# Performance work log

Hardware: AMD Instinct MI355X
Metric: run time of the kernel (lower is better)

The kernel has to match this reference:

```python
import jax, jax.numpy as jnp
import numpy as np

N_NODES = 50000
N_EDGES = 800000
N_GRAPHS = 64


def graph_conv(x, edge_index, w_rel, b_rel, w_root):
    # PyG GraphConv with aggr='add':
    #   out = lin_rel(sum_{j in N(i)} x_j) + lin_root(x_i)
    src, dst = edge_index[0], edge_index[1]
    agg = jax.ops.segment_sum(x[src], dst, num_segments=x.shape[0])  # [N, d_in]
    return agg @ w_rel + b_rel + x @ w_root  # [N, d_out]


def scatter_mean(x, batch, num_segments):
    s = jax.ops.segment_sum(x, batch, num_segments=num_segments)
    cnt = jax.ops.segment_sum(jnp.ones((x.shape[0],), x.dtype), batch,
                              num_segments=num_segments)
    return s / jnp.maximum(cnt, 1.0)[:, None]


def setup_inputs() -> dict:
    key = jax.random.key(0)
    ks = jax.random.split(key, 8)
    d_feat, d_hid, d_out = 128, 128, 128
    x = jax.random.normal(ks[0], (N_NODES, d_feat), dtype=jnp.float32)
    edge_index = jax.random.randint(ks[1], (2, N_EDGES), 0, N_NODES, dtype=jnp.int64)
    batch = jnp.sort(jax.random.randint(ks[2], (N_NODES,), 0, N_GRAPHS, dtype=jnp.int64))

    def glorot(k, shape):
        fan_in = shape[0]
        return jax.random.normal(k, shape, dtype=jnp.float32) / np.sqrt(fan_in)

    return {
        "x": x,
        "edge_index": edge_index,
        "batch": batch,
        "w_rel1": glorot(ks[3], (d_feat, d_hid)),
        "b_rel1": jnp.zeros((d_hid,), jnp.float32),
        "w_root1": glorot(ks[4], (d_feat, d_hid)),
        "w_rel2": glorot(ks[5], (d_hid, 2 * d_hid)),
        "b_rel2": jnp.zeros((2 * d_hid,), jnp.float32),
        "w_root2": glorot(ks[6], (d_hid, 2 * d_hid)),
        "w_rel3": glorot(ks[7], (2 * d_hid, d_out)),
        "b_rel3": jnp.zeros((d_out,), jnp.float32),
        "w_root3": glorot(jax.random.fold_in(key, 99), (2 * d_hid, d_out)),
    }


def reference(x, edge_index, batch,
              w_rel1, b_rel1, w_root1,
              w_rel2, b_rel2, w_root2,
              w_rel3, b_rel3, w_root3):
    h = jax.nn.elu(graph_conv(x, edge_index, w_rel1, b_rel1, w_root1))
    h = jax.nn.elu(graph_conv(h, edge_index, w_rel2, b_rel2, w_root2))
    h = jax.nn.elu(graph_conv(h, edge_index, w_rel3, b_rel3, w_root3))
    return scatter_mean(h, batch, N_GRAPHS)  # [num_graphs, n_out]
```

## Files before the change

### kernel.cpp

```cpp
#include <hip/hip_runtime.h>
#include <math.h>

#define NN 50000
#define NNP 50048
#define NE 800000
#define NG 64
#define NBK 196
#define ECH 4082
#define TOTH (NBK * NBK)
#define NBH 151
#define SBLK 6890
#define SWORK (NN * 32 + 163840)

typedef __attribute__((ext_vector_type(8))) __bf16 bf16x8;
typedef __attribute__((ext_vector_type(4))) float f32x4;

__device__ inline unsigned short f2bf(float f) {
    unsigned int u = __float_as_uint(f);
    u += 0x7fffu + ((u >> 16) & 1u);
    return (unsigned short)(u >> 16);
}
__device__ inline float bflo(unsigned int v) { return __uint_as_float(v << 16); }
__device__ inline float bfhi(unsigned int v) { return __uint_as_float(v & 0xffff0000u); }
__device__ inline float bfs(unsigned short v) { return __uint_as_float((unsigned int)v << 16); }

#define GLD_LDS16(g, l)                                                          \
    __builtin_amdgcn_global_load_lds(                                            \
        (const __attribute__((address_space(1))) unsigned int*)(g),              \
        (__attribute__((address_space(3))) unsigned int*)(l), 16, 0, 0)

__global__ __launch_bounds__(256) void front_k(const float* __restrict__ x,
                                               const float* __restrict__ wr1,
                                               const float* __restrict__ wo1,
                                               const float* __restrict__ wr2,
                                               const float* __restrict__ wo2,
                                               const float* __restrict__ wr3,
                                               const float* __restrict__ wo3,
                                               const int* __restrict__ edst,
                                               const int* __restrict__ batch,
                                               unsigned short* __restrict__ xb,
                                               unsigned short* __restrict__ W1T,
                                               unsigned short* __restrict__ W2T,
                                               unsigned short* __restrict__ W3T,
                                               int* __restrict__ H,
                                               int* __restrict__ bounds,
                                               float* __restrict__ outp) {
    const int b = blockIdx.x, t = threadIdx.x;
    if (b < SBLK) {
        int id = b * 256 + t;
        if (id < NN * 32) {
            float4 v = ((const float4*)x)[id];
            unsigned int p0 = ((unsigned int)f2bf(v.y) << 16) | f2bf(v.x);
            unsigned int p1 = ((unsigned int)f2bf(v.w) << 16) | f2bf(v.z);
            ((uint2*)xb)[id] = make_uint2(p0, p1);
            return;
        }
        int w = id - NN * 32;
        if (w < 32768) {
            int n = w >> 8, k = w & 255;
            W1T[w] = f2bf((k < 128) ? wr1[k * 128 + n] : wo1[(k - 128) * 128 + n]);
        } else if (w < 98304) {
            int j = w - 32768; int n = j >> 8, k = j & 255;
            W2T[j] = f2bf((k < 128) ? wr2[k * 256 + n] : wo2[(k - 128) * 256 + n]);
        } else if (w < 163840) {
            int j = w - 98304; int n = j >> 8, k = j & 255;
            W3T[j] = f2bf((n < 128) ? wr3[k * 128 + n] : wo3[k * 128 + (n - 128)]);
        }
        return;
    }
    if (b < SBLK + NBK) {
        __shared__ int h[NBK];
        int k = b - SBLK;
        if (t < NBK) h[t] = 0;
        __syncthreads();
        int e0 = k * ECH, e1 = min(NE, e0 + ECH);
        for (int e = e0 + t; e < e1; e += 256) atomicAdd(&h[edst[e] >> 8], 1);
        __syncthreads();
        if (t < NBK) H[t * NBK + k] = h[t];
        return;
    }
    if (t <= NG) {
        int g = t, lo = 0, hi = NN;
        while (lo < hi) { int mid = (lo + hi) >> 1; if (batch[mid] < g) lo = mid + 1; else hi = mid; }
        bounds[g] = lo;
    }
    for (int i = t; i < NG * 128; i += 256) outp[i] = 0.f;
}

__global__ __launch_bounds__(256) void hsum_k(const int* __restrict__ H,
                                              int* __restrict__ hb) {
    int i = blockIdx.x * 256 + threadIdx.x;
    int v = (i < TOTH) ? H[i] : 0;
    for (int off = 32; off; off >>= 1) v += __shfl_xor(v, off, 64);
    __shared__ int ws[4];
    if ((threadIdx.x & 63) == 0) ws[threadIdx.x >> 6] = v;
    __syncthreads();
    if (threadIdx.x == 0) hb[blockIdx.x] = ws[0] + ws[1] + ws[2] + ws[3];
}

__global__ __launch_bounds__(256) void happly_k(const int* __restrict__ H,
                                                const int* __restrict__ hb,
                                                int* __restrict__ S) {
    __shared__ int s[256], ws[4], choff;
    const int t = threadIdx.x, c = blockIdx.x;
    {
        int v = (t < c) ? hb[t] : 0;
        for (int off = 32; off; off >>= 1) v += __shfl_xor(v, off, 64);
        if ((t & 63) == 0) ws[t >> 6] = v;
        __syncthreads();
        if (t == 0) choff = ws[0] + ws[1] + ws[2] + ws[3];
        __syncthreads();
    }
    int i = c * 256 + t;
    int v = (i < TOTH) ? H[i] : 0;
    s[t] = v; __syncthreads();
    for (int off = 1; off < 256; off <<= 1) {
        int u = (t >= off) ? s[t - off] : 0;
        __syncthreads(); s[t] += u; __syncthreads();
    }
    if (i < TOTH) S[i] = choff + s[t] - v;
}

__global__ __launch_bounds__(256) void scatter_k(const int* __restrict__ src,
                                                 const int* __restrict__ dst,
                                                 const int* __restrict__ S,
                                                 int* __restrict__ tmp) {
    __shared__ int cur[NBK];
    int t = threadIdx.x, k = blockIdx.x;
    if (t < NBK) cur[t] = S[t * NBK + k];
    __syncthreads();
    int e0 = k * ECH, e1 = min(NE, e0 + ECH);
    for (int e = e0 + t; e < e1; e += 256) {
        int d = dst[e];
        int p = atomicAdd(&cur[d >> 8], 1);
        tmp[p] = ((d & 255) << 16) | src[e];
    }
}

__global__ __launch_bounds__(256) void csr_k(const int* __restrict__ tmp,
                                             const int* __restrict__ S,
                                             int* __restrict__ rowptr,
                                             int* __restrict__ colsrc) {
    __shared__ int hist[256], off[256], cur[256];
    int t = threadIdx.x, b = blockIdx.x;
    int base = S[b * NBK];
    int next = (b < NBK - 1) ? S[(b + 1) * NBK] : NE;
    int cntb = next - base;
    hist[t] = 0;
    __syncthreads();
    for (int i = t; i < cntb; i += 256) atomicAdd(&hist[tmp[base + i] >> 16], 1);
    __syncthreads();
    int v = hist[t];
    off[t] = v; __syncthreads();
    for (int o = 1; o < 256; o <<= 1) {
        int u = (t >= o) ? off[t - o] : 0;
        __syncthreads(); off[t] += u; __syncthreads();
    }
    int excl = off[t] - v;
    int node = b * 256 + t;
    if (node <= NN) rowptr[node] = base + excl;
    cur[t] = excl;
    __syncthreads();
    for (int i = t; i < cntb; i += 256) {
        int e = tmp[base + i];
        int p = atomicAdd(&cur[e >> 16], 1);
        colsrc[base + p] = e & 0xffff;
    }
}

__global__ __launch_bounds__(256) void aggb_k(const unsigned short* __restrict__ feat,
                                              const int* __restrict__ rowptr,
                                              const int* __restrict__ colsrc,
                                              unsigned short* __restrict__ outp) {
    const int node = __builtin_amdgcn_readfirstlane((int)(blockIdx.x * 4 + (threadIdx.x >> 6)));
    const int lane = threadIdx.x & 63;
    const int half = lane >> 5, l32 = lane & 31;
    const int beg = rowptr[node], end = rowptr[node + 1];
    float a0 = 0.f, a1 = 0.f, a2 = 0.f, a3 = 0.f;
    int e = beg;
    for (; e + 16 <= end; e += 16) {
        int c[8]; uint2 v[8];
#pragma unroll
        for (int i = 0; i < 8; ++i) c[i] = colsrc[e + 2 * i + half];
#pragma unroll
        for (int i = 0; i < 8; ++i)
            v[i] = *(const uint2*)&feat[(size_t)c[i] * 128 + l32 * 4];
#pragma unroll
        for (int i = 0; i < 8; ++i) {
            a0 += bflo(v[i].x); a1 += bfhi(v[i].x);
            a2 += bflo(v[i].y); a3 += bfhi(v[i].y);
        }
    }
    for (; e + 4 <= end; e += 4) {
        int c[2]; uint2 v[2];
#pragma unroll
        for (int i = 0; i < 2; ++i) c[i] = colsrc[e + 2 * i + half];
#pragma unroll
        for (int i = 0; i < 2; ++i)
            v[i] = *(const uint2*)&feat[(size_t)c[i] * 128 + l32 * 4];
#pragma unroll
        for (int i = 0; i < 2; ++i) {
            a0 += bflo(v[i].x); a1 += bfhi(v[i].x);
            a2 += bflo(v[i].y); a3 += bfhi(v[i].y);
        }
    }
    if (e + 2 <= end) {
        int c = colsrc[e + half];
        uint2 v = *(const uint2*)&feat[(size_t)c * 128 + l32 * 4];
        a0 += bflo(v.x); a1 += bfhi(v.x); a2 += bflo(v.y); a3 += bfhi(v.y);
        e += 2;
    }
    if (e < end && half == 0) {
        int c = colsrc[e];
        uint2 v = *(const uint2*)&feat[(size_t)c * 128 + l32 * 4];
        a0 += bflo(v.x); a1 += bfhi(v.x); a2 += bflo(v.y); a3 += bfhi(v.y);
    }
    a0 += __shfl_xor(a0, 32, 64);
    a1 += __shfl_xor(a1, 32, 64);
    a2 += __shfl_xor(a2, 32, 64);
    a3 += __shfl_xor(a3, 32, 64);
    if (half == 0) {
        unsigned int p0 = ((unsigned int)f2bf(a1) << 16) | f2bf(a0);
        unsigned int p1 = ((unsigned int)f2bf(a3) << 16) | f2bf(a2);
        *(uint2*)&outp[(size_t)node * 128 + l32 * 4] = make_uint2(p0, p1);
    }
}

__global__ __launch_bounds__(256) void aggf_k(const unsigned short* __restrict__ y,
                                              const unsigned short* __restrict__ rr,
                                              const float* __restrict__ b3,
                                              const int* __restrict__ rowptr,
                                              const int* __restrict__ colsrc,
                                              unsigned short* __restrict__ outp) {
    const int node = __builtin_amdgcn_readfirstlane((int)(blockIdx.x * 4 + (threadIdx.x >> 6)));
    const int lane = threadIdx.x & 63;
    const int half = lane >> 5, l32 = lane & 31;
    const int beg = rowptr[node], end = rowptr[node + 1];
    float a0 = 0.f, a1 = 0.f, a2 = 0.f, a3 = 0.f;
    int e = beg;
    for (; e + 16 <= end; e += 16) {
        int c[8]; uint2 v[8];
#pragma unroll
        for (int i = 0; i < 8; ++i) c[i] = colsrc[e + 2 * i + half];
#pragma unroll
        for (int i = 0; i < 8; ++i)
            v[i] = *(const uint2*)&y[(size_t)c[i] * 128 + l32 * 4];
#pragma unroll
        for (int i = 0; i < 8; ++i) {
            a0 += bflo(v[i].x); a1 += bfhi(v[i].x);
            a2 += bflo(v[i].y); a3 += bfhi(v[i].y);
        }
    }
    for (; e + 4 <= end; e += 4) {
        int c[2]; uint2 v[2];
#pragma unroll
        for (int i = 0; i < 2; ++i) c[i] = colsrc[e + 2 * i + half];
#pragma unroll
        for (int i = 0; i < 2; ++i)
            v[i] = *(const uint2*)&y[(size_t)c[i] * 128 + l32 * 4];
#pragma unroll
        for (int i = 0; i < 2; ++i) {
            a0 += bflo(v[i].x); a1 += bfhi(v[i].x);
            a2 += bflo(v[i].y); a3 += bfhi(v[i].y);
        }
    }
    if (e + 2 <= end) {
        int c = colsrc[e + half];
        uint2 v = *(const uint2*)&y[(size_t)c * 128 + l32 * 4];
        a0 += bflo(v.x); a1 += bfhi(v.x); a2 += bflo(v.y); a3 += bfhi(v.y);
        e += 2;
    }
    if (e < end && half == 0) {
        int c = colsrc[e];
        uint2 v = *(const uint2*)&y[(size_t)c * 128 + l32 * 4];
        a0 += bflo(v.x); a1 += bfhi(v.x); a2 += bflo(v.y); a3 += bfhi(v.y);
    }
    a0 += __shfl_xor(a0, 32, 64);
    a1 += __shfl_xor(a1, 32, 64);
    a2 += __shfl_xor(a2, 32, 64);
    a3 += __shfl_xor(a3, 32, 64);
    if (half == 0) {
        uint2 rv = *(const uint2*)&rr[(size_t)node * 128 + l32 * 4];
        float4 bb = *(const float4*)&b3[l32 * 4];
        float v0 = a0 + bflo(rv.x) + bb.x;
        float v1 = a1 + bfhi(rv.x) + bb.y;
        float v2 = a2 + bflo(rv.y) + bb.z;
        float v3 = a3 + bfhi(rv.y) + bb.w;
        v0 = v0 > 0.f ? v0 : (__expf(v0) - 1.f);
        v1 = v1 > 0.f ? v1 : (__expf(v1) - 1.f);
        v2 = v2 > 0.f ? v2 : (__expf(v2) - 1.f);
        v3 = v3 > 0.f ? v3 : (__expf(v3) - 1.f);
        unsigned int p0 = ((unsigned int)f2bf(v1) << 16) | f2bf(v0);
        unsigned int p1 = ((unsigned int)f2bf(v3) << 16) | f2bf(v2);
        *(uint2*)&outp[(size_t)node * 128 + l32 * 4] = make_uint2(p0, p1);
    }
}

template <bool TWO, int N, bool BIAS, bool ELU, bool SPLIT>
__global__ __launch_bounds__(256) void gemmB_k(const unsigned short* __restrict__ A1,
                                               const unsigned short* __restrict__ A2,
                                               const unsigned short* __restrict__ WT,
                                               const float* __restrict__ bias,
                                               unsigned short* __restrict__ Cout,
                                               unsigned short* __restrict__ Cout2) {
    constexpr int AST = TWO ? 128 : 256;
    constexpr int NH = N / 2;
    constexpr int NI = NH / 16;
    constexpr int SIT = N / 16;
    __shared__ __attribute__((aligned(16))) unsigned short Bs[N * 128];

    const int t = threadIdx.x;
    const int wv = t >> 6, lane = t & 63;
    const int qd = lane >> 4, l16 = lane & 15;
    const int m0 = blockIdx.x * 64;
    const int mrow = m0 + (wv >> 1) * 32 + l16;
    const int nb = (wv & 1) * NH;
    const int swz = (t & 15) ^ (t >> 4);

    f32x4 acc[2][NI] = {};
    bf16x8 av[2][2];

    auto stageB = [&](int p) {
#pragma unroll
        for (int i = 0; i < SIT; ++i) {
            int row = i * 16 + (t >> 4);
            const unsigned short* g = WT + (size_t)row * 256 + p * 128 + swz * 8;
            GLD_LDS16(g, &Bs[i * 2048 + t * 8]);
        }
    };
    auto loadA = [&](int ks, int d) {
        const unsigned short* base = (TWO && ks >= 4) ? A2 : A1;
        int kc = TWO ? ((ks & 3) * 32) : (ks * 32);
        av[d][0] = *(const bf16x8*)&base[(size_t)mrow * AST + kc + qd * 8];
        av[d][1] = *(const bf16x8*)&base[(size_t)(mrow + 16) * AST + kc + qd * 8];
    };
    auto kstep = [&](int ks, int d) {
        int ksl = ks & 3;
        bf16x8 bfr[NI];
#pragma unroll
        for (int ni = 0; ni < NI; ++ni) {
            int row = nb + ni * 16 + l16;
            int slot = (ksl * 4 + qd) ^ l16;
            bfr[ni] = *(const bf16x8*)&Bs[row * 128 + slot * 8];
        }
#pragma unroll
        for (int mi = 0; mi < 2; ++mi)
#pragma unroll
            for (int ni = 0; ni < NI; ++ni)
                acc[mi][ni] = __builtin_amdgcn_mfma_f32_16x16x32_bf16(
                    av[d][mi], bfr[ni], acc[mi][ni], 0, 0, 0);
    };

    stageB(0);
    asm volatile("" ::: "memory");
    loadA(0, 0);
    asm volatile("s_waitcnt vmcnt(2)" ::: "memory");
    __builtin_amdgcn_s_barrier();
    loadA(1, 1); kstep(0, 0);
    loadA(2, 0); kstep(1, 1);
    loadA(3, 1); kstep(2, 0);
    kstep(3, 1);
    asm volatile("s_waitcnt lgkmcnt(0)" ::: "memory");
    __builtin_amdgcn_s_barrier();
    stageB(1);
    asm volatile("" ::: "memory");
    loadA(4, 0);
    asm volatile("s_waitcnt vmcnt(2)" ::: "memory");
    __builtin_amdgcn_s_barrier();
    loadA(5, 1); kstep(4, 0);
    loadA(6, 0); kstep(5, 1);
    loadA(7, 1); kstep(6, 0);
    kstep(7, 1);

#pragma unroll
    for (int mi = 0; mi < 2; ++mi)
#pragma unroll
        for (int ni = 0; ni < NI; ++ni)
#pragma unroll
            for (int r = 0; r < 4; ++r) {
                int mm = m0 + (wv >> 1) * 32 + mi * 16 + qd * 4 + r;
                if (mm < NN) {
                    int nn = nb + ni * 16 + l16;
                    float v = acc[mi][ni][r];
                    if (BIAS) v += bias[nn];
                    if (ELU) v = v > 0.f ? v : (__expf(v) - 1.f);
                    unsigned short bv = f2bf(v);
                    if (SPLIT) {
                        unsigned short* dst = (nn < 128) ? Cout : Cout2;
                        dst[(size_t)mm * 128 + (nn & 127)] = bv;
                    } else {
                        Cout[(size_t)mm * N + nn] = bv;
                    }
                }
            }
}

__global__ __launch_bounds__(256) void sum_k(const unsigned short* __restrict__ vals,
                                             const int* __restrict__ batch,
                                             float* __restrict__ outsum) {
    const int CH = 25;
    int wv = threadIdx.x >> 6, lane = threadIdx.x & 63;
    int n0 = (blockIdx.x * 4 + wv) * CH;
    int g = batch[n0];
    float ax = 0.f, ay = 0.f;
    for (int i = 0; i < CH; ++i) {
        int n = n0 + i;
        int gn = batch[n];
        if (gn != g) {
            unsafeAtomicAdd(&outsum[(size_t)g * 128 + lane * 2], ax);
            unsafeAtomicAdd(&outsum[(size_t)g * 128 + lane * 2 + 1], ay);
            ax = 0.f; ay = 0.f; g = gn;
        }
        unsigned int v = *(const unsigned int*)&vals[(size_t)n * 128 + lane * 2];
        ax += bflo(v); ay += bfhi(v);
    }
    unsafeAtomicAdd(&outsum[(size_t)g * 128 + lane * 2], ax);
    unsafeAtomicAdd(&outsum[(size_t)g * 128 + lane * 2 + 1], ay);
}

__global__ void divide_k(const int* __restrict__ bounds, float* __restrict__ out) {
    int i = blockIdx.x * 256 + threadIdx.x;
    if (i < NG * 128) {
        int g = i >> 7;
        float c = (float)(bounds[g + 1] - bounds[g]);
        out[i] /= fmaxf(c, 1.f);
    }
}

extern "C" void kernel_launch(void* const* d_in, const int* in_sizes, int n_in,
                              void* d_out, int out_size, void* d_ws, size_t ws_size,
                              hipStream_t stream) {
    const float* x       = (const float*)d_in[0];
    const int*   ei      = (const int*)d_in[1];
    const int*   batch   = (const int*)d_in[2];
    const float* w_rel1  = (const float*)d_in[3];
    const float* b_rel1  = (const float*)d_in[4];
    const float* w_root1 = (const float*)d_in[5];
    const float* w_rel2  = (const float*)d_in[6];
    const float* b_rel2  = (const float*)d_in[7];
    const float* w_root2 = (const float*)d_in[8];
    const float* w_rel3  = (const float*)d_in[9];
    const float* b_rel3  = (const float*)d_in[10];
    const float* w_root3 = (const float*)d_in[11];
    const int* esrc = ei;
    const int* edst = ei + NE;

    unsigned short* Ab = (unsigned short*)d_ws;
    unsigned short* Bb = Ab + (size_t)NNP * 128;
    unsigned short* Cb = Bb + (size_t)NNP * 128;
    unsigned short* xb = Cb + (size_t)NNP * 256;
    unsigned short* W1T = xb + (size_t)NNP * 128;
    unsigned short* W2T = W1T + 128 * 256;
    unsigned short* W3T = W2T + 256 * 256;
    int* rowptr = (int*)(W3T + 256 * 256);
    int* colsrc = rowptr + (NN + 1);
    int* tmp    = colsrc + NE;
    int* H      = tmp + NE;
    int* S      = H + TOTH;
    int* hb     = S + TOTH;
    int* bounds = hb + 256;
    float* outp = (float*)d_out;

    front_k<<<SBLK + NBK + 1, 256, 0, stream>>>(
        x, w_rel1, w_root1, w_rel2, w_root2, w_rel3, w_root3, edst, batch,
        xb, W1T, W2T, W3T, H, bounds, outp);
    hsum_k<<<NBH, 256, 0, stream>>>(H, hb);
    happly_k<<<NBH, 256, 0, stream>>>(H, hb, S);
    scatter_k<<<NBK, 256, 0, stream>>>(esrc, edst, S, tmp);
    csr_k<<<NBK, 256, 0, stream>>>(tmp, S, rowptr, colsrc);

    aggb_k<<<NN / 4, 256, 0, stream>>>(xb, rowptr, colsrc, Ab);
    gemmB_k<true, 128, true, true, false>
        <<<NNP / 64, 256, 0, stream>>>(Ab, xb, W1T, b_rel1, Bb, nullptr);

    aggb_k<<<NN / 4, 256, 0, stream>>>(Bb, rowptr, colsrc, Ab);
    gemmB_k<true, 256, true, true, false>
        <<<NNP / 64, 256, 0, stream>>>(Ab, Bb, W2T, b_rel2, Cb, nullptr);

    gemmB_k<false, 256, false, false, true>
        <<<NNP / 64, 256, 0, stream>>>(Cb, nullptr, W3T, nullptr, Ab, Bb);

    aggf_k<<<NN / 4, 256, 0, stream>>>(Ab, Bb, b_rel3, rowptr, colsrc, Cb);
    sum_k<<<NN / 100, 256, 0, stream>>>(Cb, batch, outp);
    divide_k<<<(NG * 128 + 255) / 256, 256, 0, stream>>>(bounds, outp);
}
```

Measured before the change: 305.1 us.

## Slice node features into 32-column slabs for cache-friendly gather aggregation

Features are additionally written in a slab layout of four 32-column slices per node, and the aggregation kernels launch one block per node group per slice. Each block gathers only a 64-byte slice per neighbor, so the working set of each slice pass fits better in L2/MALL. Non-temporal loads and stores are used for colsrc and the outputs. The cost is extra slab writes in front_k and the GEMM epilogues, four times as many aggregation blocks, and reading colsrc four times.

```diff
diff --git a/kernel.cpp b/kernel.cpp
--- a/kernel.cpp
+++ b/kernel.cpp
@@ -39,6 +39,7 @@
                                                const int* __restrict__ edst,
                                                const int* __restrict__ batch,
                                                unsigned short* __restrict__ xb,
+                                               unsigned short* __restrict__ xs,
                                                unsigned short* __restrict__ W1T,
                                                unsigned short* __restrict__ W2T,
                                                unsigned short* __restrict__ W3T,
@@ -53,6 +54,9 @@
             unsigned int p0 = ((unsigned int)f2bf(v.y) << 16) | f2bf(v.x);
             unsigned int p1 = ((unsigned int)f2bf(v.w) << 16) | f2bf(v.z);
             ((uint2*)xb)[id] = make_uint2(p0, p1);
+            int row = id >> 5, c4 = (id & 31) << 2;
+            *(uint2*)&xs[((size_t)(c4 >> 5) * NNP + row) * 32 + (c4 & 31)] =
+                make_uint2(p0, p1);
             return;
         }
         int w = id - NN * 32;
@@ -168,141 +172,108 @@
     }
 }
 
-__global__ __launch_bounds__(256) void aggb_k(const unsigned short* __restrict__ feat,
+__global__ __launch_bounds__(256) void agg4_k(const unsigned short* __restrict__ slabs,
                                               const int* __restrict__ rowptr,
                                               const int* __restrict__ colsrc,
                                               unsigned short* __restrict__ outp) {
-    const int node = __builtin_amdgcn_readfirstlane((int)(blockIdx.x * 4 + (threadIdx.x >> 6)));
+    const int slice = blockIdx.x & 3;
+    const int node = __builtin_amdgcn_readfirstlane(
+        (int)((blockIdx.x >> 2) * 4 + (threadIdx.x >> 6)));
     const int lane = threadIdx.x & 63;
-    const int half = lane >> 5, l32 = lane & 31;
+    const int sub = lane >> 4, fl = lane & 15;
+    const unsigned short* feat = slabs + (size_t)slice * NNP * 32;
+    const int fo = fl * 2;
     const int beg = rowptr[node], end = rowptr[node + 1];
-    float a0 = 0.f, a1 = 0.f, a2 = 0.f, a3 = 0.f;
+    float a0 = 0.f, a1 = 0.f;
     int e = beg;
     for (; e + 16 <= end; e += 16) {
-        int c[8]; uint2 v[8];
-#pragma unroll
-        for (int i = 0; i < 8; ++i) c[i] = colsrc[e + 2 * i + half];
-#pragma unroll
-        for (int i = 0; i < 8; ++i)
-            v[i] = *(const uint2*)&feat[(size_t)c[i] * 128 + l32 * 4];
-#pragma unroll
-        for (int i = 0; i < 8; ++i) {
-            a0 += bflo(v[i].x); a1 += bfhi(v[i].x);
-            a2 += bflo(v[i].y); a3 += bfhi(v[i].y);
-        }
+        int c[4]; unsigned int v[4];
+#pragma unroll
+        for (int i = 0; i < 4; ++i) c[i] = __builtin_nontemporal_load(&colsrc[e + 4 * i + sub]);
+#pragma unroll
+        for (int i = 0; i < 4; ++i)
+            v[i] = *(const unsigned int*)&feat[(size_t)c[i] * 32 + fo];
+#pragma unroll
+        for (int i = 0; i < 4; ++i) { a0 += bflo(v[i]); a1 += bfhi(v[i]); }
     }
     for (; e + 4 <= end; e += 4) {
-        int c[2]; uint2 v[2];
-#pragma unroll
-        for (int i = 0; i < 2; ++i) c[i] = colsrc[e + 2 * i + half];
-#pragma unroll
-        for (int i = 0; i < 2; ++i)
-            v[i] = *(const uint2*)&feat[(size_t)c[i] * 128 + l32 * 4];
-#pragma unroll
-        for (int i = 0; i < 2; ++i) {
-            a0 += bflo(v[i].x); a1 += bfhi(v[i].x);
-            a2 += bflo(v[i].y); a3 += bfhi(v[i].y);
-        }
-    }
-    if (e + 2 <= end) {
-        int c = colsrc[e + half];
-        uint2 v = *(const uint2*)&feat[(size_t)c * 128 + l32 * 4];
-        a0 += bflo(v.x); a1 += bfhi(v.x); a2 += bflo(v.y); a3 += bfhi(v.y);
-        e += 2;
-    }
-    if (e < end && half == 0) {
-        int c = colsrc[e];
-        uint2 v = *(const uint2*)&feat[(size_t)c * 128 + l32 * 4];
-        a0 += bflo(v.x); a1 += bfhi(v.x); a2 += bflo(v.y); a3 += bfhi(v.y);
-    }
-    a0 += __shfl_xor(a0, 32, 64);
-    a1 += __shfl_xor(a1, 32, 64);
-    a2 += __shfl_xor(a2, 32, 64);
-    a3 += __shfl_xor(a3, 32, 64);
-    if (half == 0) {
-        unsigned int p0 = ((unsigned int)f2bf(a1) << 16) | f2bf(a0);
-        unsigned int p1 = ((unsigned int)f2bf(a3) << 16) | f2bf(a2);
-        *(uint2*)&outp[(size_t)node * 128 + l32 * 4] = make_uint2(p0, p1);
-    }
-}
-
-__global__ __launch_bounds__(256) void aggf_k(const unsigned short* __restrict__ y,
-                                              const unsigned short* __restrict__ rr,
-                                              const float* __restrict__ b3,
-                                              const int* __restrict__ rowptr,
-                                              const int* __restrict__ colsrc,
-                                              unsigned short* __restrict__ outp) {
-    const int node = __builtin_amdgcn_readfirstlane((int)(blockIdx.x * 4 + (threadIdx.x >> 6)));
+        int c = __builtin_nontemporal_load(&colsrc[e + sub]);
+        unsigned int v = *(const unsigned int*)&feat[(size_t)c * 32 + fo];
+        a0 += bflo(v); a1 += bfhi(v);
+    }
+    int rem = end - e;
+    if (sub < rem) {
+        int c = __builtin_nontemporal_load(&colsrc[e + sub]);
+        unsigned int v = *(const unsigned int*)&feat[(size_t)c * 32 + fo];
+        a0 += bflo(v); a1 += bfhi(v);
+    }
+    a0 += __shfl_xor(a0, 16, 64); a1 += __shfl_xor(a1, 16, 64);
+    a0 += __shfl_xor(a0, 32, 64); a1 += __shfl_xor(a1, 32, 64);
+    if (lane < 16) {
+        unsigned int p = ((unsigned int)f2bf(a1) << 16) | f2bf(a0);
+        __builtin_nontemporal_store(p, (unsigned int*)&outp[(size_t)node * 128 + slice * 32 + fo]);
+    }
+}
+
+__global__ __launch_bounds__(256) void aggf4_k(const unsigned short* __restrict__ slabs,
+                                               const unsigned short* __restrict__ rr,
+                                               const float* __restrict__ b3,
+                                               const int* __restrict__ rowptr,
+                                               const int* __restrict__ colsrc,
+                                               unsigned short* __restrict__ outp) {
+    const int slice = blockIdx.x & 3;
+    const int node = __builtin_amdgcn_readfirstlane(
+        (int)((blockIdx.x >> 2) * 4 + (threadIdx.x >> 6)));
     const int lane = threadIdx.x & 63;
-    const int half = lane >> 5, l32 = lane & 31;
+    const int sub = lane >> 4, fl = lane & 15;
+    const unsigned short* feat = slabs + (size_t)slice * NNP * 32;
+    const int fo = fl * 2;
     const int beg = rowptr[node], end = rowptr[node + 1];
-    float a0 = 0.f, a1 = 0.f, a2 = 0.f, a3 = 0.f;
+    float a0 = 0.f, a1 = 0.f;
     int e = beg;
     for (; e + 16 <= end; e += 16) {
-        int c[8]; uint2 v[8];
-#pragma unroll
-        for (int i = 0; i < 8; ++i) c[i] = colsrc[e + 2 * i + half];
-#pragma unroll
-        for (int i = 0; i < 8; ++i)
-            v[i] = *(const uint2*)&y[(size_t)c[i] * 128 + l32 * 4];
-#pragma unroll
-        for (int i = 0; i < 8; ++i) {
-            a0 += bflo(v[i].x); a1 += bfhi(v[i].x);
-            a2 += bflo(v[i].y); a3 += bfhi(v[i].y);
-        }
+        int c[4]; unsigned int v[4];
+#pragma unroll
+        for (int i = 0; i < 4; ++i) c[i] = __builtin_nontemporal_load(&colsrc[e + 4 * i + sub]);
+#pragma unroll
+        for (int i = 0; i < 4; ++i)
+            v[i] = *(const unsigned int*)&feat[(size_t)c[i] * 32 + fo];
+#pragma unroll
+        for (int i = 0; i < 4; ++i) { a0 += bflo(v[i]); a1 += bfhi(v[i]); }
     }
     for (; e + 4 <= end; e += 4) {
-        int c[2]; uint2 v[2];
-#pragma unroll
-        for (int i = 0; i < 2; ++i) c[i] = colsrc[e + 2 * i + half];
-#pragma unroll
-        for (int i = 0; i < 2; ++i)
-            v[i] = *(const uint2*)&y[(size_t)c[i] * 128 + l32 * 4];
-#pragma unroll
-        for (int i = 0; i < 2; ++i) {
-            a0 += bflo(v[i].x); a1 += bfhi(v[i].x);
-            a2 += bflo(v[i].y); a3 += bfhi(v[i].y);
-        }
-    }
-    if (e + 2 <= end) {
-        int c = colsrc[e + half];
-        uint2 v = *(const uint2*)&y[(size_t)c * 128 + l32 * 4];
-        a0 += bflo(v.x); a1 += bfhi(v.x); a2 += bflo(v.y); a3 += bfhi(v.y);
-        e += 2;
-    }
-    if (e < end && half == 0) {
-        int c = colsrc[e];
-        uint2 v = *(const uint2*)&y[(size_t)c * 128 + l32 * 4];
-        a0 += bflo(v.x); a1 += bfhi(v.x); a2 += bflo(v.y); a3 += bfhi(v.y);
-    }
-    a0 += __shfl_xor(a0, 32, 64);
-    a1 += __shfl_xor(a1, 32, 64);
-    a2 += __shfl_xor(a2, 32, 64);
-    a3 += __shfl_xor(a3, 32, 64);
-    if (half == 0) {
-        uint2 rv = *(const uint2*)&rr[(size_t)node * 128 + l32 * 4];
-        float4 bb = *(const float4*)&b3[l32 * 4];
-        float v0 = a0 + bflo(rv.x) + bb.x;
-        float v1 = a1 + bfhi(rv.x) + bb.y;
-        float v2 = a2 + bflo(rv.y) + bb.z;
-        float v3 = a3 + bfhi(rv.y) + bb.w;
+        int c = __builtin_nontemporal_load(&colsrc[e + sub]);
+        unsigned int v = *(const unsigned int*)&feat[(size_t)c * 32 + fo];
+        a0 += bflo(v); a1 += bfhi(v);
+    }
+    int rem = end - e;
+    if (sub < rem) {
+        int c = __builtin_nontemporal_load(&colsrc[e + sub]);
+        unsigned int v = *(const unsigned int*)&feat[(size_t)c * 32 + fo];
+        a0 += bflo(v); a1 += bfhi(v);
+    }
+    a0 += __shfl_xor(a0, 16, 64); a1 += __shfl_xor(a1, 16, 64);
+    a0 += __shfl_xor(a0, 32, 64); a1 += __shfl_xor(a1, 32, 64);
+    if (lane < 16) {
+        int col = slice * 32 + fo;
+        unsigned int rv = *(const unsigned int*)&rr[(size_t)node * 128 + col];
+        float2 bb = *(const float2*)&b3[col];
+        float v0 = a0 + bflo(rv) + bb.x;
+        float v1 = a1 + bfhi(rv) + bb.y;
         v0 = v0 > 0.f ? v0 : (__expf(v0) - 1.f);
         v1 = v1 > 0.f ? v1 : (__expf(v1) - 1.f);
-        v2 = v2 > 0.f ? v2 : (__expf(v2) - 1.f);
-        v3 = v3 > 0.f ? v3 : (__expf(v3) - 1.f);
-        unsigned int p0 = ((unsigned int)f2bf(v1) << 16) | f2bf(v0);
-        unsigned int p1 = ((unsigned int)f2bf(v3) << 16) | f2bf(v2);
-        *(uint2*)&outp[(size_t)node * 128 + l32 * 4] = make_uint2(p0, p1);
-    }
-}
-
-template <bool TWO, int N, bool BIAS, bool ELU, bool SPLIT>
+        unsigned int p = ((unsigned int)f2bf(v1) << 16) | f2bf(v0);
+        __builtin_nontemporal_store(p, (unsigned int*)&outp[(size_t)node * 128 + col]);
+    }
+}
+
+template <bool TWO, int N, bool BIAS, bool ELU, int SLAB>
 __global__ __launch_bounds__(256) void gemmB_k(const unsigned short* __restrict__ A1,
                                                const unsigned short* __restrict__ A2,
                                                const unsigned short* __restrict__ WT,
                                                const float* __restrict__ bias,
                                                unsigned short* __restrict__ Cout,
-                                               unsigned short* __restrict__ Cout2) {
+                                               unsigned short* __restrict__ slab) {
     constexpr int AST = TWO ? 128 : 256;
     constexpr int NH = N / 2;
     constexpr int NI = NH / 16;
@@ -385,11 +356,15 @@
                     if (BIAS) v += bias[nn];
                     if (ELU) v = v > 0.f ? v : (__expf(v) - 1.f);
                     unsigned short bv = f2bf(v);
-                    if (SPLIT) {
-                        unsigned short* dst = (nn < 128) ? Cout : Cout2;
-                        dst[(size_t)mm * 128 + (nn & 127)] = bv;
+                    if (SLAB == 2) {
+                        if (nn < 128)
+                            slab[((size_t)(nn >> 5) * NNP + mm) * 32 + (nn & 31)] = bv;
+                        else
+                            Cout[(size_t)mm * 128 + (nn & 127)] = bv;
                     } else {
                         Cout[(size_t)mm * N + nn] = bv;
+                        if (SLAB == 1)
+                            slab[((size_t)(nn >> 5) * NNP + mm) * 32 + (nn & 31)] = bv;
                     }
                 }
             }
@@ -449,7 +424,9 @@
     unsigned short* Bb = Ab + (size_t)NNP * 128;
     unsigned short* Cb = Bb + (size_t)NNP * 128;
     unsigned short* xb = Cb + (size_t)NNP * 256;
-    unsigned short* W1T = xb + (size_t)NNP * 128;
+    unsigned short* xs = xb + (size_t)NNP * 128;
+    unsigned short* hs = xs + (size_t)NNP * 128;
+    unsigned short* W1T = hs + (size_t)NNP * 128;
     unsigned short* W2T = W1T + 128 * 256;
     unsigned short* W3T = W2T + 256 * 256;
     int* rowptr = (int*)(W3T + 256 * 256);
@@ -459,28 +436,29 @@
     int* S      = H + TOTH;
     int* hb     = S + TOTH;
     int* bounds = hb + 256;
+    unsigned short* ys = xs;
     float* outp = (float*)d_out;
 
     front_k<<<SBLK + NBK + 1, 256, 0, stream>>>(
         x, w_rel1, w_root1, w_rel2, w_root2, w_rel3, w_root3, edst, batch,
-        xb, W1T, W2T, W3T, H, bounds, outp);
+        xb, xs, W1T, W2T, W3T, H, bounds, outp);
     hsum_k<<<NBH, 256, 0, stream>>>(H, hb);
     happly_k<<<NBH, 256, 0, stream>>>(H, hb, S);
     scatter_k<<<NBK, 256, 0, stream>>>(esrc, edst, S, tmp);
     csr_k<<<NBK, 256, 0, stream>>>(tmp, S, rowptr, colsrc);
 
-    aggb_k<<<NN / 4, 256, 0, stream>>>(xb, rowptr, colsrc, Ab);
-    gemmB_k<true, 128, true, true, false>
-        <<<NNP / 64, 256, 0, stream>>>(Ab, xb, W1T, b_rel1, Bb, nullptr);
-
-    aggb_k<<<NN / 4, 256, 0, stream>>>(Bb, rowptr, colsrc, Ab);
-    gemmB_k<true, 256, true, true, false>
+    agg4_k<<<NN, 256, 0, stream>>>(xs, rowptr, colsrc, Ab);
+    gemmB_k<true, 128, true, true, 1>
+        <<<NNP / 64, 256, 0, stream>>>(Ab, xb, W1T, b_rel1, Bb, hs);
+
+    agg4_k<<<NN, 256, 0, stream>>>(hs, rowptr, colsrc, Ab);
+    gemmB_k<true, 256, true, true, 0>
         <<<NNP / 64, 256, 0, stream>>>(Ab, Bb, W2T, b_rel2, Cb, nullptr);
 
-    gemmB_k<false, 256, false, false, true>
-        <<<NNP / 64, 256, 0, stream>>>(Cb, nullptr, W3T, nullptr, Ab, Bb);
-
-    aggf_k<<<NN / 4, 256, 0, stream>>>(Ab, Bb, b_rel3, rowptr, colsrc, Cb);
+    gemmB_k<false, 256, false, false, 2>
+        <<<NNP / 64, 256, 0, stream>>>(Cb, nullptr, W3T, nullptr, Bb, ys);
+
+    aggf4_k<<<NN, 256, 0, stream>>>(ys, Bb, b_rel3, rowptr, colsrc, Cb);
     sum_k<<<NN / 100, 256, 0, stream>>>(Cb, batch, outp);
     divide_k<<<(NG * 128 + 255) / 256, 256, 0, stream>>>(bounds, outp);
 }
```

New measurement: 473.8 us. 1.55x slower.

## Restructure GEMM into 128-row tiles with full-K weight slab staged once

Applied to the files above, without the earlier changes.

Replaces the two-phase pipelined GEMM kernel with one where each block handles 128 rows and one 128-column output half, loads all K=256 of its A fragments into registers up front, and stages the entire 128x256 weight slice into LDS in a single pass. Wider outputs are split across paired blocks. The goal is fewer barriers and phase switches, and more rows reusing each staged weight tile. In exchange it uses more registers and 64KB of LDS per block, and it no longer overlaps loads with MFMA work inside a block.

```diff
diff --git a/kernel.cpp b/kernel.cpp
--- a/kernel.cpp
+++ b/kernel.cpp
@@ -10,7 +10,6 @@
 #define TOTH (NBK * NBK)
 #define NBH 151
 #define SBLK 6890
-#define SWORK (NN * 32 + 163840)
 
 typedef __attribute__((ext_vector_type(8))) __bf16 bf16x8;
 typedef __attribute__((ext_vector_type(4))) float f32x4;
@@ -296,100 +295,83 @@
     }
 }
 
-template <bool TWO, int N, bool BIAS, bool ELU, bool SPLIT>
-__global__ __launch_bounds__(256) void gemmB_k(const unsigned short* __restrict__ A1,
-                                               const unsigned short* __restrict__ A2,
-                                               const unsigned short* __restrict__ WT,
-                                               const float* __restrict__ bias,
-                                               unsigned short* __restrict__ Cout,
-                                               unsigned short* __restrict__ Cout2) {
+template <bool TWO, int NOUT, bool BIAS, bool ELU, bool SPLIT>
+__global__ __launch_bounds__(256, 2) void gemmS_k(const unsigned short* __restrict__ A1,
+                                                  const unsigned short* __restrict__ A2,
+                                                  const unsigned short* __restrict__ WT,
+                                                  const float* __restrict__ bias,
+                                                  unsigned short* __restrict__ C1,
+                                                  unsigned short* __restrict__ C2) {
+    constexpr int NH = NOUT / 128;
     constexpr int AST = TWO ? 128 : 256;
-    constexpr int NH = N / 2;
-    constexpr int NI = NH / 16;
-    constexpr int SIT = N / 16;
-    __shared__ __attribute__((aligned(16))) unsigned short Bs[N * 128];
+    __shared__ __attribute__((aligned(16))) unsigned short Ws[128 * 256];
 
     const int t = threadIdx.x;
     const int wv = t >> 6, lane = t & 63;
     const int qd = lane >> 4, l16 = lane & 15;
-    const int m0 = blockIdx.x * 64;
-    const int mrow = m0 + (wv >> 1) * 32 + l16;
-    const int nb = (wv & 1) * NH;
-    const int swz = (t & 15) ^ (t >> 4);
-
-    f32x4 acc[2][NI] = {};
-    bf16x8 av[2][2];
-
-    auto stageB = [&](int p) {
-#pragma unroll
-        for (int i = 0; i < SIT; ++i) {
-            int row = i * 16 + (t >> 4);
-            const unsigned short* g = WT + (size_t)row * 256 + p * 128 + swz * 8;
-            GLD_LDS16(g, &Bs[i * 2048 + t * 8]);
-        }
-    };
-    auto loadA = [&](int ks, int d) {
+    const int h  = (NH == 2) ? (int)(blockIdx.x & 1) : 0;
+    const int rb = (NH == 2) ? (int)(blockIdx.x >> 1) : (int)blockIdx.x;
+    const int m0 = rb * 128;
+    const int mrow = m0 + wv * 32 + l16;
+
+    bf16x8 av[16];
+#pragma unroll
+    for (int ks = 0; ks < 8; ++ks) {
         const unsigned short* base = (TWO && ks >= 4) ? A2 : A1;
-        int kc = TWO ? ((ks & 3) * 32) : (ks * 32);
-        av[d][0] = *(const bf16x8*)&base[(size_t)mrow * AST + kc + qd * 8];
-        av[d][1] = *(const bf16x8*)&base[(size_t)(mrow + 16) * AST + kc + qd * 8];
-    };
-    auto kstep = [&](int ks, int d) {
-        int ksl = ks & 3;
-        bf16x8 bfr[NI];
-#pragma unroll
-        for (int ni = 0; ni < NI; ++ni) {
-            int row = nb + ni * 16 + l16;
-            int slot = (ksl * 4 + qd) ^ l16;
-            bfr[ni] = *(const bf16x8*)&Bs[row * 128 + slot * 8];
+        const int kc = TWO ? ((ks & 3) * 32) : (ks * 32);
+        av[2 * ks]     = *(const bf16x8*)&base[(size_t)mrow * AST + kc + qd * 8];
+        av[2 * ks + 1] = *(const bf16x8*)&base[(size_t)(mrow + 16) * AST + kc + qd * 8];
+    }
+    {
+        const int rl = t >> 5;
+        const int slot = t & 31;
+#pragma unroll
+        for (int i = 0; i < 16; ++i) {
+            int r = i * 8 + rl;
+            const unsigned short* g =
+                WT + (size_t)(h * 128 + r) * 256 + ((slot ^ (r & 15)) * 8);
+            GLD_LDS16(g, &Ws[i * 2048 + t * 8]);
+        }
+    }
+    asm volatile("s_waitcnt vmcnt(0)" ::: "memory");
+    __builtin_amdgcn_s_barrier();
+
+    f32x4 acc[2][8] = {};
+#pragma unroll
+    for (int ks = 0; ks < 8; ++ks) {
+        bf16x8 bfr[8];
+#pragma unroll
+        for (int ni = 0; ni < 8; ++ni) {
+            int r = ni * 16 + l16;
+            int slot = (ks * 4 + qd) ^ l16;
+            bfr[ni] = *(const bf16x8*)&Ws[r * 256 + slot * 8];
         }
 #pragma unroll
         for (int mi = 0; mi < 2; ++mi)
 #pragma unroll
-            for (int ni = 0; ni < NI; ++ni)
+            for (int ni = 0; ni < 8; ++ni)
                 acc[mi][ni] = __builtin_amdgcn_mfma_f32_16x16x32_bf16(
-                    av[d][mi], bfr[ni], acc[mi][ni], 0, 0, 0);
-    };
-
-    stageB(0);
-    asm volatile("" ::: "memory");
-    loadA(0, 0);
-    asm volatile("s_waitcnt vmcnt(2)" ::: "memory");
-    __builtin_amdgcn_s_barrier();
-    loadA(1, 1); kstep(0, 0);
-    loadA(2, 0); kstep(1, 1);
-    loadA(3, 1); kstep(2, 0);
-    kstep(3, 1);
-    asm volatile("s_waitcnt lgkmcnt(0)" ::: "memory");
-    __builtin_amdgcn_s_barrier();
-    stageB(1);
-    asm volatile("" ::: "memory");
-    loadA(4, 0);
-    asm volatile("s_waitcnt vmcnt(2)" ::: "memory");
-    __builtin_amdgcn_s_barrier();
-    loadA(5, 1); kstep(4, 0);
-    loadA(6, 0); kstep(5, 1);
-    loadA(7, 1); kstep(6, 0);
-    kstep(7, 1);
+                    av[2 * ks + mi], bfr[ni], acc[mi][ni], 0, 0, 0);
+    }
 
 #pragma unroll
     for (int mi = 0; mi < 2; ++mi)
 #pragma unroll
-        for (int ni = 0; ni < NI; ++ni)
+        for (int ni = 0; ni < 8; ++ni)
 #pragma unroll
             for (int r = 0; r < 4; ++r) {
-                int mm = m0 + (wv >> 1) * 32 + mi * 16 + qd * 4 + r;
+                int mm = m0 + wv * 32 + mi * 16 + qd * 4 + r;
                 if (mm < NN) {
-                    int nn = nb + ni * 16 + l16;
+                    int nn = ni * 16 + l16;
                     float v = acc[mi][ni][r];
-                    if (BIAS) v += bias[nn];
+                    if (BIAS) v += bias[h * 128 + nn];
                     if (ELU) v = v > 0.f ? v : (__expf(v) - 1.f);
                     unsigned short bv = f2bf(v);
                     if (SPLIT) {
-                        unsigned short* dst = (nn < 128) ? Cout : Cout2;
-                        dst[(size_t)mm * 128 + (nn & 127)] = bv;
+                        unsigned short* dst = h ? C2 : C1;
+                        dst[(size_t)mm * 128 + nn] = bv;
                     } else {
-                        Cout[(size_t)mm * N + nn] = bv;
+                        C1[(size_t)mm * NOUT + h * 128 + nn] = bv;
                     }
                 }
             }
@@ -470,15 +452,15 @@
     csr_k<<<NBK, 256, 0, stream>>>(tmp, S, rowptr, colsrc);
 
     aggb_k<<<NN / 4, 256, 0, stream>>>(xb, rowptr, colsrc, Ab);
-    gemmB_k<true, 128, true, true, false>
-        <<<NNP / 64, 256, 0, stream>>>(Ab, xb, W1T, b_rel1, Bb, nullptr);
+    gemmS_k<true, 128, true, true, false>
+        <<<NNP / 128, 256, 0, stream>>>(Ab, xb, W1T, b_rel1, Bb, nullptr);
 
     aggb_k<<<NN / 4, 256, 0, stream>>>(Bb, rowptr, colsrc, Ab);
-    gemmB_k<true, 256, true, true, false>
-        <<<NNP / 64, 256, 0, stream>>>(Ab, Bb, W2T, b_rel2, Cb, nullptr);
-
-    gemmB_k<false, 256, false, false, true>
-        <<<NNP / 64, 256, 0, stream>>>(Cb, nullptr, W3T, nullptr, Ab, Bb);
+    gemmS_k<true, 256, true, true, false>
+        <<<2 * (NNP / 128), 256, 0, stream>>>(Ab, Bb, W2T, b_rel2, Cb, nullptr);
+
+    gemmS_k<false, 256, false, false, true>
+        <<<2 * (NNP / 128), 256, 0, stream>>>(Cb, nullptr, W3T, nullptr, Ab, Bb);
 
     aggf_k<<<NN / 4, 256, 0, stream>>>(Ab, Bb, b_rel3, rowptr, colsrc, Cb);
     sum_k<<<NN / 100, 256, 0, stream>>>(Cb, batch, outp);
```

Result: no change. 307.5 us (+0.8%).
